# Performance work log

Measured on AMD Instinct MI355X. Metric: run time of the kernel, lower is better.

## Reference

```python
import jax, jax.numpy as jnp
import numpy as np


def setup_inputs() -> dict:
    key = jax.random.key(0)
    k1, k2 = jax.random.split(key)
    B, Tq, Ts, H = 16, 2048, 2048, 1024
    hidden = jax.random.normal(k1, (B, Tq, H), dtype=jnp.float32)
    encoder_outputs = jax.random.normal(k2, (B, Ts, H), dtype=jnp.float32)
    return {"hidden": hidden, "encoder_outputs": encoder_outputs}


def reference(hidden, encoder_outputs):
    # scores[b, s, q] = <encoder_outputs[b, s], hidden[b, q]>  (no scaling)
    scores = jnp.einsum("bsh,bqh->bsq", encoder_outputs, hidden)
    # softmax over the source dimension s (dim=1, the NON-last axis)
    attn_weights = jax.nn.softmax(scores, axis=1)
    # context[b, q, h] = sum_s attn[b, s, q] * enc[b, s, h]
    context = jnp.einsum("bsq,bsh->bqh", attn_weights, encoder_outputs)
    return context
```

## Files before the change

### kernel.cpp

```cpp
#include <hip/hip_runtime.h>

#define NB_ 16
#define TQ_ 2048
#define TS_ 2048
#define DH_ 1024
#define QB_ 32
#define SB_ 256
#define NT_ 512
#define VTS_ 80

typedef _Float16 f16x8 __attribute__((ext_vector_type(8)));
typedef _Float16 f16x4 __attribute__((ext_vector_type(4)));
typedef float f32x4 __attribute__((ext_vector_type(4)));

#define LDS_BARRIER() asm volatile("s_waitcnt lgkmcnt(0)\n\ts_barrier" ::: "memory")

__device__ inline uint32_t pack_h2(float a, float b) {
  union { _Float16 h[2]; uint32_t u; } c;
  c.h[0] = (_Float16)a; c.h[1] = (_Float16)b;
  return c.u;
}

__global__ void convert_f32_f16(const float* __restrict__ src, _Float16* __restrict__ dst) {
  size_t i = ((size_t)blockIdx.x * blockDim.x + threadIdx.x) * 8;
  float4 v0 = *(const float4*)(src + i);
  float4 v1 = *(const float4*)(src + i + 4);
  f16x8 o;
  o[0] = (_Float16)v0.x; o[1] = (_Float16)v0.y; o[2] = (_Float16)v0.z; o[3] = (_Float16)v0.w;
  o[4] = (_Float16)v1.x; o[5] = (_Float16)v1.y; o[6] = (_Float16)v1.z; o[7] = (_Float16)v1.w;
  *(f16x8*)(dst + i) = o;
}

__device__ inline f16x8 cvt8(const float* __restrict__ fp) {
  float4 a = *(const float4*)fp;
  float4 b = *(const float4*)(fp + 4);
  f16x8 t;
  t[0] = (_Float16)a.x; t[1] = (_Float16)a.y; t[2] = (_Float16)a.z; t[3] = (_Float16)a.w;
  t[4] = (_Float16)b.x; t[5] = (_Float16)b.y; t[6] = (_Float16)b.z; t[7] = (_Float16)b.w;
  return t;
}

template<bool WS16>
__device__ inline f16x8 ld8(const _Float16* __restrict__ hp, const float* __restrict__ fp, size_t idx) {
  if constexpr (WS16) return *(const f16x8*)(hp + idx);
  else return cvt8(fp + idx);
}

template<bool WS16>
__global__ __launch_bounds__(NT_, 2)
void attn_v16(const float* __restrict__ hid,
              const float* __restrict__ enc,
              const _Float16* __restrict__ encH,
              float* __restrict__ out) {
  __shared__ __attribute__((aligned(16))) char smem[156544];
  char*  const q_base = smem;
  float* const s_lds  = (float*)(smem + 65536);
  char*  const p_base = smem + 98816;
  char*  const vt_all = smem + 115200;
  float* const m_lds  = (float*)(smem + 156160);
  float* const l_lds  = m_lds + 32;
  float* const c_lds  = m_lds + 64;

  const int tid  = threadIdx.x;
  const int lane = tid & 63;
  const int wid  = tid >> 6;
  const int arow = lane & 15;
  const int agrp = lane >> 4;

  const int bi  = blockIdx.x;
  const int x   = bi & 7;
  const int idx = bi >> 3;
  const int b   = x + 8 * (idx >> 6);
  const int q0  = (idx & 63) * QB_;

  const int hw = wid;

  if (tid < 32) { m_lds[tid] = -__builtin_inff(); l_lds[tid] = 0.0f; }

  {
    const float* qsrc = hid + ((size_t)b * TQ_ + q0) * DH_;
    #pragma unroll
    for (int k = 0; k < 16; ++k) {
      int i = tid + k * NT_;
      int q = i >> 8;
      int h = (i & 255) * 4;
      float4 v = *(const float4*)(qsrc + (size_t)q * DH_ + h);
      int byte = (q * 2048 + h * 2) ^ ((q & 7) << 4);
      *(uint32_t*)(q_base + byte)     = pack_h2(v.x, v.y);
      *(uint32_t*)(q_base + byte + 4) = pack_h2(v.z, v.w);
    }
  }
  __syncthreads();

  f32x4 o_acc[2][8];
  #pragma unroll
  for (int m = 0; m < 2; ++m)
    #pragma unroll
    for (int n = 0; n < 8; ++n)
      o_acc[m][n] = {};

  char* const vt = vt_all + wid * 5120;
  const size_t enc_b = (size_t)b * TS_ * DH_;
  const int c8 = (lane & 7) * 8;
  const int d2 = (lane >> 3) * 2;

  for (int st = 0; st < TS_ / SB_; ++st) {
    const int s0 = st * SB_;

    f32x4 sacc[2][2] = {{{}, {}}, {{}, {}}};
    {
      const size_t krow = enc_b + (size_t)(s0 + wid * 32 + arow) * DH_;
      #pragma unroll
      for (int kf = 0; kf < 32; ++kf) {
        const int d = kf * 32 + agrp * 8;
        f16x8 bf0 = ld8<WS16>(encH, enc, krow + d);
        f16x8 bf1 = ld8<WS16>(encH, enc, krow + (size_t)16 * DH_ + d);
        f16x8 af0 = *(const f16x8*)(q_base + ((arow * 2048 + d * 2) ^ ((arow & 7) << 4)));
        f16x8 af1 = *(const f16x8*)(q_base + (((16 + arow) * 2048 + d * 2) ^ ((arow & 7) << 4)));
        sacc[0][0] = __builtin_amdgcn_mfma_f32_16x16x32_f16(af0, bf0, sacc[0][0], 0, 0, 0);
        sacc[0][1] = __builtin_amdgcn_mfma_f32_16x16x32_f16(af0, bf1, sacc[0][1], 0, 0, 0);
        sacc[1][0] = __builtin_amdgcn_mfma_f32_16x16x32_f16(af1, bf0, sacc[1][0], 0, 0, 0);
        sacc[1][1] = __builtin_amdgcn_mfma_f32_16x16x32_f16(af1, bf1, sacc[1][1], 0, 0, 0);
      }
    }

    f16x8 stgA[2][2], stgB[2][2];
    #pragma unroll
    for (int it = 0; it < 2; ++it) {
      size_t base = enc_b + (size_t)(s0 + it * 16 + d2) * DH_ + hw * 128 + c8;
      stgA[it][0] = ld8<WS16>(encH, enc, base);
      stgA[it][1] = ld8<WS16>(encH, enc, base + DH_);
    }

    {
      const int sc = wid * 32 + arow;
      #pragma unroll
      for (int m = 0; m < 2; ++m)
        #pragma unroll
        for (int n = 0; n < 2; ++n)
          #pragma unroll
          for (int i2 = 0; i2 < 4; ++i2)
            s_lds[(m * 16 + agrp * 4 + i2) * 260 + sc + n * 16] = sacc[m][n][i2];
    }

    LDS_BARRIER();

    {
      int q = tid >> 4, sq = tid & 15;
      const float* bp = s_lds + q * 260 + sq * 16;
      f32x4 v0 = *(const f32x4*)bp;
      f32x4 v1 = *(const f32x4*)(bp + 4);
      f32x4 v2 = *(const f32x4*)(bp + 8);
      f32x4 v3 = *(const f32x4*)(bp + 12);
      f32x4 vm = v0;
      #pragma unroll
      for (int j = 0; j < 4; ++j) { vm[j] = fmaxf(fmaxf(v0[j], v1[j]), fmaxf(v2[j], v3[j])); }
      float mx = fmaxf(fmaxf(vm[0], vm[1]), fmaxf(vm[2], vm[3]));
      #pragma unroll
      for (int o = 8; o; o >>= 1) mx = fmaxf(mx, __shfl_xor(mx, o));
      float mprev = m_lds[q];
      float mnew  = fmaxf(mprev, mx);
      float p[16], ps = 0.0f;
      #pragma unroll
      for (int j = 0; j < 4; ++j) {
        p[j]      = __expf(v0[j] - mnew);
        p[4 + j]  = __expf(v1[j] - mnew);
        p[8 + j]  = __expf(v2[j] - mnew);
        p[12 + j] = __expf(v3[j] - mnew);
      }
      #pragma unroll
      for (int j = 0; j < 16; ++j) ps += p[j];
      #pragma unroll
      for (int o = 8; o; o >>= 1) ps += __shfl_xor(ps, o);
      if (sq == 0) {
        float cf = __expf(mprev - mnew);
        m_lds[q] = mnew;
        l_lds[q] = l_lds[q] * cf + ps;
        c_lds[q] = cf;
      }
      #pragma unroll
      for (int g2 = 0; g2 < 2; ++g2) {
        f16x8 pw;
        #pragma unroll
        for (int j = 0; j < 8; ++j) pw[j] = (_Float16)p[g2 * 8 + j];
        *(f16x8*)(p_base + ((q * 512 + sq * 32 + g2 * 16) ^ ((q & 7) << 4))) = pw;
      }
    }

    LDS_BARRIER();

    #pragma unroll
    for (int m = 0; m < 2; ++m)
      #pragma unroll
      for (int i2 = 0; i2 < 4; ++i2) {
        float cf = c_lds[m * 16 + agrp * 4 + i2];
        #pragma unroll
        for (int n = 0; n < 8; ++n) o_acc[m][n][i2] *= cf;
      }

    #pragma unroll
    for (int pass = 0; pass < 16; ++pass) {
      const int r  = pass >> 3, sp = pass & 7;
      const bool useA = (pass & 1) == 0;
      #pragma unroll
      for (int it = 0; it < 2; ++it) {
        int sl = it * 16 + d2;
        #pragma unroll
        for (int jj = 0; jj < 8; ++jj) {
          int hl = c8 + jj;
          union { _Float16 h[2]; uint32_t u; } pk;
          pk.h[0] = useA ? stgA[it][0][jj] : stgB[it][0][jj];
          pk.h[1] = useA ? stgA[it][1][jj] : stgB[it][1][jj];
          *(uint32_t*)(vt + ((hl * VTS_ + sl * 2) ^ (((hl >> 3) & 7) << 4))) = pk.u;
        }
      }
      if (pass < 15) {
        const int rn = (pass + 1) >> 3, spn = (pass + 1) & 7;
        #pragma unroll
        for (int it = 0; it < 2; ++it) {
          size_t base = enc_b + (size_t)(s0 + spn * 32 + it * 16 + d2) * DH_
                        + hw * 128 + rn * 64 + c8;
          if (useA) {
            stgB[it][0] = ld8<WS16>(encH, enc, base);
            stgB[it][1] = ld8<WS16>(encH, enc, base + DH_);
          } else {
            stgA[it][0] = ld8<WS16>(encH, enc, base);
            stgA[it][1] = ld8<WS16>(encH, enc, base + DH_);
          }
        }
      }
      f16x8 paf0 = *(const f16x8*)(p_base +
          ((arow * 512 + sp * 64 + agrp * 16) ^ ((arow & 7) << 4)));
      f16x8 paf1 = *(const f16x8*)(p_base +
          (((16 + arow) * 512 + sp * 64 + agrp * 16) ^ ((arow & 7) << 4)));
      __builtin_amdgcn_s_setprio(1);
      #pragma unroll
      for (int n = 0; n < 4; ++n) {
        int hl = n * 16 + arow;
        f16x8 bv = *(const f16x8*)(vt + ((hl * VTS_ + agrp * 16) ^ (((hl >> 3) & 7) << 4)));
        o_acc[0][r * 4 + n] = __builtin_amdgcn_mfma_f32_16x16x32_f16(paf0, bv, o_acc[0][r * 4 + n], 0, 0, 0);
        o_acc[1][r * 4 + n] = __builtin_amdgcn_mfma_f32_16x16x32_f16(paf1, bv, o_acc[1][r * 4 + n], 0, 0, 0);
      }
      __builtin_amdgcn_s_setprio(0);
    }
  }

  #pragma unroll
  for (int m = 0; m < 2; ++m) {
    #pragma unroll
    for (int i2 = 0; i2 < 4; ++i2) {
      int qr = m * 16 + agrp * 4 + i2;
      float inv = 1.0f / l_lds[qr];
      #pragma unroll
      for (int n = 0; n < 8; ++n) {
        out[((size_t)(b * TQ_ + q0 + qr)) * DH_ + hw * 128 + (n >> 2) * 64 + (n & 3) * 16 + arow] =
            o_acc[m][n][i2] * inv;
      }
    }
  }
}

extern "C" void kernel_launch(void* const* d_in, const int* in_sizes, int n_in,
                              void* d_out, int out_size, void* d_ws, size_t ws_size,
                              hipStream_t stream) {
  (void)in_sizes; (void)n_in; (void)out_size;
  const float* hid = (const float*)d_in[0];
  const float* enc = (const float*)d_in[1];
  float* out = (float*)d_out;

  const size_t encN = (size_t)NB_ * TS_ * DH_;
  const bool ws16 = (ws_size >= encN * sizeof(_Float16));

  dim3 grid(NB_ * (TQ_ / QB_), 1, 1);
  dim3 block(NT_, 1, 1);

  if (ws16) {
    _Float16* encH = (_Float16*)d_ws;
    convert_f32_f16<<<dim3((unsigned)(encN / 8 / 256)), dim3(256), 0, stream>>>(enc, encH);
    attn_v16<true><<<grid, block, 0, stream>>>(hid, enc, encH, out);
  } else {
    attn_v16<false><<<grid, block, 0, stream>>>(hid, enc, nullptr, out);
  }
}
```

Measured before the change: 755.2 us.

## Load V tiles directly to LDS and read transposed with ds_read_b64_tr_b16

In the fp16 workspace path, the PV stage no longer stages V through registers and transposes it with scalar LDS stores. It issues global_load_lds DMA copies into a per-wave double buffer, then uses the hardware transpose LDS read (ds_read_b64_tr_b16) to form MFMA B operands. Explicit vmcnt/lgkmcnt waits and sched barriers pipeline this. The goal is to remove VGPR staging and many small LDS writes, and to shrink LDS use. The risk is exposed load latency from the tight per-pass waits, and the output column mapping changes to match the new layout.

```diff
diff --git a/kernel.cpp b/kernel.cpp
--- a/kernel.cpp
+++ b/kernel.cpp
@@ -7,7 +7,6 @@
 #define QB_ 32
 #define SB_ 256
 #define NT_ 512
-#define VTS_ 80
 
 typedef _Float16 f16x8 __attribute__((ext_vector_type(8)));
 typedef _Float16 f16x4 __attribute__((ext_vector_type(4)));
@@ -46,18 +45,37 @@
   else return cvt8(fp + idx);
 }
 
+typedef __attribute__((address_space(1))) const void g1void;
+typedef __attribute__((address_space(3))) void l3void;
+__device__ inline void gload_lds16(const void* g, void* l) {
+  __builtin_amdgcn_global_load_lds((g1void*)g, (l3void*)l, 16, 0, 0);
+}
+__device__ inline uint32_t lds_off(void* p) {
+  return (uint32_t)(size_t)(__attribute__((address_space(3))) char*)p;
+}
+__device__ inline f16x4 tr_read(uint32_t addr) {
+  f16x4 d;
+  asm volatile("ds_read_b64_tr_b16 %0, %1" : "=v"(d) : "v"(addr));
+  return d;
+}
+__device__ inline f16x4 tr_read_o128(uint32_t addr) {
+  f16x4 d;
+  asm volatile("ds_read_b64_tr_b16 %0, %1 offset:128" : "=v"(d) : "v"(addr));
+  return d;
+}
+
 template<bool WS16>
 __global__ __launch_bounds__(NT_, 2)
-void attn_v16(const float* __restrict__ hid,
+void attn_v17(const float* __restrict__ hid,
               const float* __restrict__ enc,
               const _Float16* __restrict__ encH,
               float* __restrict__ out) {
-  __shared__ __attribute__((aligned(16))) char smem[156544];
+  __shared__ __attribute__((aligned(16))) char smem[148352];
   char*  const q_base = smem;
   float* const s_lds  = (float*)(smem + 65536);
   char*  const p_base = smem + 98816;
   char*  const vt_all = smem + 115200;
-  float* const m_lds  = (float*)(smem + 156160);
+  float* const m_lds  = (float*)(smem + 147968);
   float* const l_lds  = m_lds + 32;
   float* const c_lds  = m_lds + 64;
 
@@ -99,13 +117,19 @@
     for (int n = 0; n < 8; ++n)
       o_acc[m][n] = {};
 
-  char* const vt = vt_all + wid * 5120;
+  char* const vtb = vt_all + wid * 4096;
   const size_t enc_b = (size_t)b * TS_ * DH_;
-  const int c8 = (lane & 7) * 8;
-  const int d2 = (lane >> 3) * 2;
 
   for (int st = 0; st < TS_ / SB_; ++st) {
     const int s0 = st * SB_;
+
+    auto issueV = [&](int pass, int buf) {
+      const int sp = pass >> 2, hh = pass & 3;
+      const _Float16* g0 = encH + enc_b + (size_t)(s0 + sp * 32 + (lane >> 1)) * DH_
+                           + hw * 128 + hh * 32 + (lane & 1) * 8;
+      gload_lds16(g0,      vtb + buf * 2048);
+      gload_lds16(g0 + 16, vtb + buf * 2048 + 1024);
+    };
 
     f32x4 sacc[2][2] = {{{}, {}}, {{}, {}}};
     {
@@ -124,12 +148,9 @@
       }
     }
 
-    f16x8 stgA[2][2], stgB[2][2];
-    #pragma unroll
-    for (int it = 0; it < 2; ++it) {
-      size_t base = enc_b + (size_t)(s0 + it * 16 + d2) * DH_ + hw * 128 + c8;
-      stgA[it][0] = ld8<WS16>(encH, enc, base);
-      stgA[it][1] = ld8<WS16>(encH, enc, base + DH_);
+    if constexpr (WS16) {
+      issueV(0, 0);
+      issueV(1, 1);
     }
 
     {
@@ -198,50 +219,91 @@
         for (int n = 0; n < 8; ++n) o_acc[m][n][i2] *= cf;
       }
 
-    #pragma unroll
-    for (int pass = 0; pass < 16; ++pass) {
-      const int r  = pass >> 3, sp = pass & 7;
-      const bool useA = (pass & 1) == 0;
+    if constexpr (WS16) {
+      f16x8 paf0 = {}, paf1 = {};
+      #pragma unroll
+      for (int pass = 0; pass < 32; ++pass) {
+        const int sp = pass >> 2, hh = pass & 3;
+        const int buf = pass & 1;
+        if ((pass & 3) == 0) {
+          paf0 = *(const f16x8*)(p_base +
+              ((arow * 512 + sp * 64 + agrp * 16) ^ ((arow & 7) << 4)));
+          paf1 = *(const f16x8*)(p_base +
+              (((16 + arow) * 512 + sp * 64 + agrp * 16) ^ ((arow & 7) << 4)));
+        }
+        if (pass < 31) asm volatile("s_waitcnt vmcnt(2)" ::: "memory");
+        else           asm volatile("s_waitcnt vmcnt(0)" ::: "memory");
+        __builtin_amdgcn_sched_barrier(0);
+        const uint32_t vb = lds_off(vtb + buf * 2048) + agrp * 256 + arow * 8;
+        f16x4 b0lo = tr_read(vb);
+        f16x4 b0hi = tr_read_o128(vb);
+        f16x4 b1lo = tr_read(vb + 1024);
+        f16x4 b1hi = tr_read_o128(vb + 1024);
+        asm volatile("s_waitcnt lgkmcnt(0)" ::: "memory");
+        __builtin_amdgcn_sched_barrier(0);
+        if (pass < 30) issueV(pass + 2, buf);
+        f16x8 bv0, bv1;
+        #pragma unroll
+        for (int j = 0; j < 4; ++j) {
+          bv0[j] = b0lo[j]; bv0[4 + j] = b0hi[j];
+          bv1[j] = b1lo[j]; bv1[4 + j] = b1hi[j];
+        }
+        __builtin_amdgcn_s_setprio(1);
+        o_acc[0][hh * 2 + 0] = __builtin_amdgcn_mfma_f32_16x16x32_f16(paf0, bv0, o_acc[0][hh * 2 + 0], 0, 0, 0);
+        o_acc[1][hh * 2 + 0] = __builtin_amdgcn_mfma_f32_16x16x32_f16(paf1, bv0, o_acc[1][hh * 2 + 0], 0, 0, 0);
+        o_acc[0][hh * 2 + 1] = __builtin_amdgcn_mfma_f32_16x16x32_f16(paf0, bv1, o_acc[0][hh * 2 + 1], 0, 0, 0);
+        o_acc[1][hh * 2 + 1] = __builtin_amdgcn_mfma_f32_16x16x32_f16(paf1, bv1, o_acc[1][hh * 2 + 1], 0, 0, 0);
+        __builtin_amdgcn_s_setprio(0);
+      }
+    } else {
+      char* const vt = vtb;
+      const int c8 = (lane & 7) * 8;
+      const int d2 = (lane >> 3) * 2;
+      f16x8 stgA[2][2], stgB[2][2];
       #pragma unroll
       for (int it = 0; it < 2; ++it) {
-        int sl = it * 16 + d2;
-        #pragma unroll
-        for (int jj = 0; jj < 8; ++jj) {
-          int hl = c8 + jj;
-          union { _Float16 h[2]; uint32_t u; } pk;
-          pk.h[0] = useA ? stgA[it][0][jj] : stgB[it][0][jj];
-          pk.h[1] = useA ? stgA[it][1][jj] : stgB[it][1][jj];
-          *(uint32_t*)(vt + ((hl * VTS_ + sl * 2) ^ (((hl >> 3) & 7) << 4))) = pk.u;
-        }
-      }
-      if (pass < 15) {
-        const int rn = (pass + 1) >> 3, spn = (pass + 1) & 7;
+        size_t base = enc_b + (size_t)(s0 + it * 16 + d2) * DH_ + hw * 128 + c8;
+        stgA[it][0] = ld8<WS16>(encH, enc, base);
+        stgA[it][1] = ld8<WS16>(encH, enc, base + DH_);
+      }
+      #pragma unroll
+      for (int pass = 0; pass < 16; ++pass) {
+        const int r = pass >> 3, sp = pass & 7;
+        const bool useA = (pass & 1) == 0;
         #pragma unroll
         for (int it = 0; it < 2; ++it) {
-          size_t base = enc_b + (size_t)(s0 + spn * 32 + it * 16 + d2) * DH_
-                        + hw * 128 + rn * 64 + c8;
-          if (useA) {
-            stgB[it][0] = ld8<WS16>(encH, enc, base);
-            stgB[it][1] = ld8<WS16>(encH, enc, base + DH_);
-          } else {
-            stgA[it][0] = ld8<WS16>(encH, enc, base);
-            stgA[it][1] = ld8<WS16>(encH, enc, base + DH_);
+          int sl = it * 16 + d2;
+          #pragma unroll
+          for (int jj = 0; jj < 8; ++jj) {
+            int hl = c8 + jj;
+            union { _Float16 h[2]; uint32_t u; } pk;
+            pk.h[0] = useA ? stgA[it][0][jj] : stgB[it][0][jj];
+            pk.h[1] = useA ? stgA[it][1][jj] : stgB[it][1][jj];
+            *(uint32_t*)(vt + ((hl * 64 + sl * 2) ^ (((hl >> 3) & 7) << 4))) = pk.u;
           }
         }
-      }
-      f16x8 paf0 = *(const f16x8*)(p_base +
-          ((arow * 512 + sp * 64 + agrp * 16) ^ ((arow & 7) << 4)));
-      f16x8 paf1 = *(const f16x8*)(p_base +
-          (((16 + arow) * 512 + sp * 64 + agrp * 16) ^ ((arow & 7) << 4)));
-      __builtin_amdgcn_s_setprio(1);
-      #pragma unroll
-      for (int n = 0; n < 4; ++n) {
-        int hl = n * 16 + arow;
-        f16x8 bv = *(const f16x8*)(vt + ((hl * VTS_ + agrp * 16) ^ (((hl >> 3) & 7) << 4)));
-        o_acc[0][r * 4 + n] = __builtin_amdgcn_mfma_f32_16x16x32_f16(paf0, bv, o_acc[0][r * 4 + n], 0, 0, 0);
-        o_acc[1][r * 4 + n] = __builtin_amdgcn_mfma_f32_16x16x32_f16(paf1, bv, o_acc[1][r * 4 + n], 0, 0, 0);
-      }
-      __builtin_amdgcn_s_setprio(0);
+        if (pass < 15) {
+          const int rn = (pass + 1) >> 3, spn = (pass + 1) & 7;
+          #pragma unroll
+          for (int it = 0; it < 2; ++it) {
+            size_t base = enc_b + (size_t)(s0 + spn * 32 + it * 16 + d2) * DH_
+                          + hw * 128 + rn * 64 + c8;
+            if (useA) { stgB[it][0] = ld8<WS16>(encH, enc, base); stgB[it][1] = ld8<WS16>(encH, enc, base + DH_); }
+            else      { stgA[it][0] = ld8<WS16>(encH, enc, base); stgA[it][1] = ld8<WS16>(encH, enc, base + DH_); }
+          }
+        }
+        f16x8 paf0 = *(const f16x8*)(p_base +
+            ((arow * 512 + sp * 64 + agrp * 16) ^ ((arow & 7) << 4)));
+        f16x8 paf1 = *(const f16x8*)(p_base +
+            (((16 + arow) * 512 + sp * 64 + agrp * 16) ^ ((arow & 7) << 4)));
+        #pragma unroll
+        for (int n = 0; n < 4; ++n) {
+          int hl = n * 16 + arow;
+          f16x8 bv = *(const f16x8*)(vt + ((hl * 64 + agrp * 16) ^ (((hl >> 3) & 7) << 4)));
+          o_acc[0][r * 4 + n] = __builtin_amdgcn_mfma_f32_16x16x32_f16(paf0, bv, o_acc[0][r * 4 + n], 0, 0, 0);
+          o_acc[1][r * 4 + n] = __builtin_amdgcn_mfma_f32_16x16x32_f16(paf1, bv, o_acc[1][r * 4 + n], 0, 0, 0);
+        }
+      }
     }
   }
 
@@ -253,7 +315,7 @@
       float inv = 1.0f / l_lds[qr];
       #pragma unroll
       for (int n = 0; n < 8; ++n) {
-        out[((size_t)(b * TQ_ + q0 + qr)) * DH_ + hw * 128 + (n >> 2) * 64 + (n & 3) * 16 + arow] =
+        out[((size_t)(b * TQ_ + q0 + qr)) * DH_ + hw * 128 + (n >> 1) * 32 + (n & 1) * 16 + arow] =
             o_acc[m][n][i2] * inv;
       }
     }
@@ -277,8 +339,8 @@
   if (ws16) {
     _Float16* encH = (_Float16*)d_ws;
     convert_f32_f16<<<dim3((unsigned)(encN / 8 / 256)), dim3(256), 0, stream>>>(enc, encH);
-    attn_v16<true><<<grid, block, 0, stream>>>(hid, enc, encH, out);
+    attn_v17<true><<<grid, block, 0, stream>>>(hid, enc, encH, out);
   } else {
-    attn_v16<false><<<grid, block, 0, stream>>>(hid, enc, nullptr, out);
+    attn_v17<false><<<grid, block, 0, stream>>>(hid, enc, nullptr, out);
   }
 }
```

New measurement: 786.9 us. +4.2%, slower.
